# Performance work log

Measured on AMD Instinct MI355X. Metric: run time of the kernel, lower is better.

Reference implementation:

```python
import jax, jax.numpy as jnp
import numpy as np

B, H, W, R, C = 4, 64, 64, 64, 32  # batch, height, width, in-channels r, conv out-channels


def setup_inputs() -> dict:
    key = jax.random.key(0)
    kx, kf, kg = jax.random.split(key, 3)
    x = jax.random.normal(kx, (B, H, W, R), dtype=jnp.float32)
    # 1x1 conv with in_channels=1: kernel is effectively a length-C vector
    w_f = jax.random.normal(kf, (C,), dtype=jnp.float32) * 0.1
    w_g = jax.random.normal(kg, (C,), dtype=jnp.float32) * 0.1
    gamma = jnp.ones((), dtype=jnp.float32)
    return {"x": x, "w_f": w_f, "w_g": w_g, "gamma": gamma}


def reference(x, w_f, w_g, gamma):
    b, h, w, r = x.shape
    hw = h * w
    xs = x.reshape(b, hw, r)                      # [B, HW, R]
    # conv_f / conv_g: each scalar of xs times weight vector -> [B, HW, R*C]
    x_f = (xs[..., None] * w_f).reshape(b, hw, -1)
    x_g = (xs[..., None] * w_g).reshape(b, hw, -1)
    attn = jnp.einsum('bik,bjk->bij', x_f, x_g)   # [B, HW, HW]
    attn = jax.nn.softmax(attn, axis=-1) * gamma
    # out[b,j,r] = sum_i attn[b,j,i] * xs[b,i,r]
    out = jnp.einsum('bji,bir->bjr', attn, xs)
    return out.reshape(b, h, w, r)
```

## Files before the change

### kernel.cpp

```cpp
#include <hip/hip_runtime.h>


#define N_SEQ 4096
#define KS    4
#define LOG2E 1.4426950408889634f
#define LDP2  72

typedef __attribute__((ext_vector_type(8))) short short8;
typedef __attribute__((ext_vector_type(4))) short short4v;
typedef __attribute__((ext_vector_type(4))) float f4;
typedef _Float16 half8  __attribute__((ext_vector_type(8)));
typedef _Float16 half4v __attribute__((ext_vector_type(4)));
typedef _Float16 half2t __attribute__((ext_vector_type(2)));
typedef __fp16   fp16x2 __attribute__((ext_vector_type(2)));

union U8  { short8 v8; short4v v4[2]; unsigned short u[8]; };
union HU8 { half8 v; half2t h2[4]; unsigned short u[8]; };
union HU4 { half4v v; half2t h2[2]; unsigned short u[4]; };
union PK  { fp16x2 f; half2t h; };

#define MFMA16(a,b,c) __builtin_amdgcn_mfma_f32_16x16x32_bf16(a,b,c,0,0,0)
#define MFMAH(a,b,c)  __builtin_amdgcn_mfma_f32_16x16x32_f16(a,b,c,0,0,0)

static __device__ __forceinline__ unsigned short f2bf(float f){
  unsigned int u = __float_as_uint(f);
  u += 0x7fffu + ((u>>16)&1u);
  return (unsigned short)(u>>16);
}
static __device__ __forceinline__ float bf2f(unsigned short b){
  return __uint_as_float(((unsigned int)b)<<16);
}
static __device__ __forceinline__ half2t pkrtz(float a, float b){
#if __has_builtin(__builtin_amdgcn_cvt_pkrtz)
  PK u; u.f = __builtin_amdgcn_cvt_pkrtz(a, b);
  return u.h;
#else
  half2t r; r.x = (_Float16)a; r.y = (_Float16)b; return r;
#endif
}
static __device__ __forceinline__ float fexp2(float x){
#if __has_builtin(__builtin_amdgcn_exp2f)
  return __builtin_amdgcn_exp2f(x);
#else
  return exp2f(x);
#endif
}
static __device__ __forceinline__ f4 splat4(float v){ f4 r; r.x=v; r.y=v; r.z=v; r.w=v; return r; }
static __device__ __forceinline__ f4 exp2v(f4 v){
  f4 r; r.x=fexp2(v.x); r.y=fexp2(v.y); r.z=fexp2(v.z); r.w=fexp2(v.w); return r;
}
static __device__ __forceinline__ f4 max4(f4 a, f4 b){
  f4 r; r.x=fmaxf(a.x,b.x); r.y=fmaxf(a.y,b.y); r.z=fmaxf(a.z,b.z); r.w=fmaxf(a.w,b.w); return r;
}
static __device__ __forceinline__ f4 shx4(f4 v, int m){
  f4 r; r.x=__shfl_xor(v.x,m,64); r.y=__shfl_xor(v.y,m,64);
        r.z=__shfl_xor(v.z,m,64); r.w=__shfl_xor(v.w,m,64); return r;
}
static __device__ __forceinline__ void gld_lds16(const void* g, void* l){
  __builtin_amdgcn_global_load_lds(
      (const __attribute__((address_space(1))) unsigned int*)g,
      (__attribute__((address_space(3))) unsigned int*)l, 16, 0, 0);
}

__global__ __launch_bounds__(256) void prep_kernel(
    const float* __restrict__ x, unsigned short* __restrict__ xh,
    unsigned short* __restrict__ xt)
{
  __shared__ unsigned short T[64][66];
  const int tid = threadIdx.x;
  const int bb  = blockIdx.x >> 6;
  const int n0  = (blockIdx.x & 63) << 6;
  {
    const int r  = tid >> 2;
    const int c4 = tid & 3;
    const float* src = x + ((size_t)(bb*N_SEQ + n0 + r))*64 + c4*16;
    unsigned short h[16];
    #pragma unroll
    for (int i = 0; i < 4; ++i) {
      const float4 f = *(const float4*)(src + i*4);
      HU4 u; u.h2[0] = pkrtz(f.x, f.y); u.h2[1] = pkrtz(f.z, f.w);
      h[i*4+0]=u.u[0]; h[i*4+1]=u.u[1]; h[i*4+2]=u.u[2]; h[i*4+3]=u.u[3];
    }
    unsigned short* dst = xh + ((size_t)(bb*N_SEQ + n0 + r))*64 + c4*16;
    U8 u0, u1;
    #pragma unroll
    for (int j = 0; j < 8; ++j) { u0.u[j]=h[j]; u1.u[j]=h[8+j]; }
    *(short8*)dst = u0.v8; *(short8*)(dst+8) = u1.v8;
    #pragma unroll
    for (int j = 0; j < 16; ++j) T[r][c4*16+j] = h[j];
  }
  __syncthreads();
  {
    const int d = tid >> 2;
    const int g = tid & 3;
    unsigned short o[16];
    #pragma unroll
    for (int j = 0; j < 16; ++j) o[j] = T[g*16+j][d];
    unsigned short* dst = xt + ((size_t)(bb*64 + d))*N_SEQ + n0 + g*16;
    U8 u0, u1;
    #pragma unroll
    for (int j = 0; j < 8; ++j) { u0.u[j]=o[j]; u1.u[j]=o[8+j]; }
    *(short8*)dst = u0.v8; *(short8*)(dst+8) = u1.v8;
  }
}

__global__ __launch_bounds__(256, 3) void fattn2_kernel(
    const float* __restrict__ x, const float* __restrict__ wf,
    const float* __restrict__ wg,
    const unsigned short* __restrict__ xh, const unsigned short* __restrict__ xt,
    float* __restrict__ OP, float* __restrict__ LP)
{
  __shared__ __align__(16) unsigned short KH[2][4096];
  __shared__ __align__(16) unsigned short VT[2][4096];
  __shared__ __align__(16) unsigned short PB[4][32*LDP2];

  const int tid  = threadIdx.x;
  const int lane = tid & 63;
  const int wv   = tid >> 6;
  const int mg   = wv & 1;
  const int hh   = wv >> 1;
  const int quad = lane >> 4;
  const int l15  = lane & 15;
  const int swz  = l15 & 7;
  const int ks   = blockIdx.x >> 8;
  const int rem  = blockIdx.x & 255;
  const int bb   = rem >> 6;
  const int qb   = (rem & 63) << 6;

  float s = 0.f;
  #pragma unroll
  for (int i = 0; i < 32; ++i) s += wf[i]*wg[i];
  const float s2 = s * LOG2E;

  const float* xb = x + ((size_t)bb * N_SEQ) * 64;

  half8 qf[2][2];
  #pragma unroll
  for (int mt = 0; mt < 2; ++mt) {
    const int row = qb + mg*32 + mt*16 + l15;
    #pragma unroll
    for (int c = 0; c < 2; ++c) {
      const float* src = xb + row*64 + c*32 + quad*8;
      const float4 a0 = *(const float4*)src;
      const float4 a1 = *(const float4*)(src+4);
      HU8 u;
      u.h2[0] = pkrtz(a0.x*s2, a0.y*s2);
      u.h2[1] = pkrtz(a0.z*s2, a0.w*s2);
      u.h2[2] = pkrtz(a1.x*s2, a1.y*s2);
      u.h2[3] = pkrtz(a1.z*s2, a1.w*s2);
      qf[mt][c] = u.v;
    }
  }

  f4 Oc[2][4];
  f4 lsa[2];
  #pragma unroll
  for (int mt = 0; mt < 2; ++mt) {
    lsa[mt] = splat4(0.f);
    #pragma unroll
    for (int nt = 0; nt < 4; ++nt) Oc[mt][nt] = splat4(0.f);
  }

  const int kbb = ks*1024;
  unsigned short* PBw = PB[wv];

  #pragma unroll 1
  for (int t = 0; t < 8; ++t) {
    const int kt = kbb + t*64;
    #pragma unroll
    for (int i = 0; i < 8; ++i) {
      const int reg = i >> 1;
      const int h   = reg & 1;
      const int ch  = wv*2 + (i & 1);
      const int p   = ch*64 + lane;
      const int rr  = p >> 3;
      const int cg  = (p & 7) ^ (rr & 7);
      if (reg < 2) {
        gld_lds16(xh + ((size_t)(bb*N_SEQ + kt + h*512 + rr))*64 + cg*8, &KH[h][ch*512]);
      } else {
        gld_lds16(xt + ((size_t)(bb*64 + rr))*N_SEQ + (kt + h*512 + cg*8), &VT[h][ch*512]);
      }
    }
    __syncthreads();

    f4 St[4][2];
    #pragma unroll
    for (int k2 = 0; k2 < 4; ++k2)
      #pragma unroll
      for (int mt = 0; mt < 2; ++mt) St[k2][mt] = splat4(0.f);

    #pragma unroll
    for (int c = 0; c < 2; ++c) {
      half8 kf[4];
      #pragma unroll
      for (int k2 = 0; k2 < 4; ++k2)
        kf[k2] = *(const half8*)&KH[hh][(k2*16 + l15)*64 + (((c*4 + quad) ^ swz))*8];
      #pragma unroll
      for (int k2 = 0; k2 < 4; ++k2)
        #pragma unroll
        for (int mt = 0; mt < 2; ++mt)
          St[k2][mt] = MFMAH(kf[k2], qf[mt][c], St[k2][mt]);
    }

    #pragma unroll
    for (int k2 = 0; k2 < 4; ++k2) {
      #pragma unroll
      for (int mt = 0; mt < 2; ++mt) {
        const f4 p = exp2v(St[k2][mt]);
        lsa[mt] += p;
        HU4 u; u.h2[0] = pkrtz(p.x, p.y); u.h2[1] = pkrtz(p.z, p.w);
        *(half4v*)&PBw[(mt*16 + l15)*LDP2 + k2*16 + quad*4] = u.v;
      }
    }

    #pragma unroll
    for (int kc = 0; kc < 2; ++kc) {
      half8 pa[2];
      #pragma unroll
      for (int mt = 0; mt < 2; ++mt)
        pa[mt] = *(const half8*)&PBw[(mt*16 + l15)*LDP2 + kc*32 + quad*8];
      #pragma unroll
      for (int nt = 0; nt < 4; ++nt) {
        const half8 vb = *(const half8*)&VT[hh][(nt*16 + l15)*64 + (((kc*4 + quad) ^ swz))*8];
        #pragma unroll
        for (int mt = 0; mt < 2; ++mt)
          Oc[mt][nt] = MFMAH(pa[mt], vb, Oc[mt][nt]);
      }
    }
    __syncthreads();
  }

  float lsum[2];
  #pragma unroll
  for (int mt = 0; mt < 2; ++mt) {
    float sv = lsa[mt].x + lsa[mt].y + lsa[mt].z + lsa[mt].w;
    sv += __shfl_xor(sv, 16, 64);
    sv += __shfl_xor(sv, 32, 64);
    lsum[mt] = sv;
  }

  float* MO = (float*)KH;
  float* ML = (float*)VT;
  if (hh == 1) {
    #pragma unroll
    for (int mt = 0; mt < 2; ++mt) {
      const int rbase = mg*32 + mt*16 + quad*4;
      #pragma unroll
      for (int nt = 0; nt < 4; ++nt) {
        MO[(rbase+0)*64 + nt*16 + l15] = Oc[mt][nt].x;
        MO[(rbase+1)*64 + nt*16 + l15] = Oc[mt][nt].y;
        MO[(rbase+2)*64 + nt*16 + l15] = Oc[mt][nt].z;
        MO[(rbase+3)*64 + nt*16 + l15] = Oc[mt][nt].w;
      }
      if (quad == 0) ML[mg*32 + mt*16 + l15] = lsum[mt];
    }
  }
  __syncthreads();
  if (hh == 0) {
    float* op = OP + (size_t)blockIdx.x * 4096;
    #pragma unroll
    for (int mt = 0; mt < 2; ++mt) {
      const int rbase = mg*32 + mt*16 + quad*4;
      #pragma unroll
      for (int nt = 0; nt < 4; ++nt) {
        #pragma unroll
        for (int rg = 0; rg < 4; ++rg) {
          const int rr = rbase + rg;
          op[rr*64 + nt*16 + l15] = Oc[mt][nt][rg] + MO[rr*64 + nt*16 + l15];
        }
      }
      if (quad == 0)
        LP[(size_t)blockIdx.x*64 + mg*32 + mt*16 + l15] = lsum[mt] + ML[mg*32 + mt*16 + l15];
    }
  }
}

__global__ __launch_bounds__(256) void merge_kernel(
    const float* __restrict__ OP, const float* __restrict__ LP,
    const float* __restrict__ gm, float* __restrict__ out)
{
  const int idx = blockIdx.x*256 + threadIdx.x;
  const int e0  = idx*4;
  const int d0  = e0 & 63;
  const int row = e0 >> 6;
  const int bb  = row >> 12;
  const int q   = row & 4095;
  const int qt  = q >> 6;
  const int qr  = q & 63;
  float4 acc = make_float4(0.f,0.f,0.f,0.f);
  float l = 0.f;
  #pragma unroll
  for (int sct = 0; sct < KS; ++sct) {
    const int blk = sct*256 + bb*64 + qt;
    const float4 o = *(const float4*)(OP + (size_t)blk*4096 + qr*64 + d0);
    acc.x += o.x; acc.y += o.y; acc.z += o.z; acc.w += o.w;
    l += LP[(size_t)blk*64 + qr];
  }
  const float w = gm[0] / l;
  float4 r; r.x = acc.x*w; r.y = acc.y*w; r.z = acc.z*w; r.w = acc.w*w;
  *(float4*)(out + e0) = r;
}

#define LDKF 72
#define TILEF (64*LDKF)
#define LDP 36

__global__ __launch_bounds__(256) void fattn_fallback(
    const float* __restrict__ x, const float* __restrict__ wf,
    const float* __restrict__ wg, const float* __restrict__ gm,
    float* __restrict__ out)
{
  __shared__ __align__(16) unsigned short KHI[2*TILEF];
  __shared__ __align__(16) unsigned short KLO[2*TILEF];
  __shared__ __align__(16) unsigned short VT [2*TILEF];
  __shared__ __align__(16) unsigned short PB [4*32*LDP];

  const int tid  = threadIdx.x;
  const int lane = tid & 63;
  const int wv   = tid >> 6;
  const int mg   = wv & 1;
  const int hh   = wv >> 1;
  const int quad = lane >> 4;
  const int l15  = lane & 15;
  const int bb   = blockIdx.x >> 6;
  const int qb   = (blockIdx.x & 63) << 6;

  float s = 0.f;
  #pragma unroll
  for (int i = 0; i < 32; ++i) s += wf[i]*wg[i];
  const float s2 = s * LOG2E;
  const float gamma = gm[0];

  const float* xb = x + ((size_t)bb * N_SEQ) * 64;

  short8 qhf[2][2], qlf[2][2];
  #pragma unroll
  for (int mt = 0; mt < 2; ++mt) {
    const int row = qb + mg*32 + mt*16 + l15;
    #pragma unroll
    for (int c = 0; c < 2; ++c) {
      const float* src = xb + row*64 + c*32 + quad*8;
      const float4 a0 = *(const float4*)src;
      const float4 a1 = *(const float4*)(src+4);
      float qv[8] = {a0.x,a0.y,a0.z,a0.w,a1.x,a1.y,a1.z,a1.w};
      U8 vh, vl;
      #pragma unroll
      for (int j = 0; j < 8; ++j) {
        float q = qv[j]*s2;
        unsigned short hb = f2bf(q);
        vh.u[j] = (short)hb;
        vl.u[j] = (short)f2bf(q - bf2f(hb));
      }
      qhf[mt][c] = vh.v8; qlf[mt][c] = vl.v8;
    }
  }

  f4 Oc[2][4], mo[2], ls[2];
  #pragma unroll
  for (int mt = 0; mt < 2; ++mt) {
    mo[mt] = splat4(-1e30f);
    ls[mt] = splat4(0.f);
    #pragma unroll
    for (int nt = 0; nt < 4; ++nt) Oc[mt][nt] = splat4(0.f);
  }

  const int sh   = tid >> 7;
  const int srow = (tid & 127) >> 1;
  const int sch  = tid & 1;

  float4 sr[8];
  {
    const float* sp = xb + (sh*2048 + srow)*64 + sch*32;
    #pragma unroll
    for (int i = 0; i < 8; ++i) sr[i] = *(const float4*)(sp + i*4);
    unsigned short hb[32], lb[32];
    #pragma unroll
    for (int i = 0; i < 8; ++i) {
      float vv[4] = {sr[i].x, sr[i].y, sr[i].z, sr[i].w};
      #pragma unroll
      for (int j = 0; j < 4; ++j) {
        unsigned short h = f2bf(vv[j]);
        hb[i*4+j] = h;
        lb[i*4+j] = f2bf(vv[j] - bf2f(h));
      }
    }
    const int kbase = sh*TILEF + srow*LDKF + sch*32;
    #pragma unroll
    for (int g = 0; g < 4; ++g) {
      U8 wh, wl;
      #pragma unroll
      for (int j = 0; j < 8; ++j) { wh.u[j]=(short)hb[g*8+j]; wl.u[j]=(short)lb[g*8+j]; }
      *(short8*)&KHI[kbase+g*8] = wh.v8;
      *(short8*)&KLO[kbase+g*8] = wl.v8;
    }
    #pragma unroll
    for (int j = 0; j < 32; ++j) VT[sh*TILEF + (sch*32+j)*LDKF + srow] = hb[j];
  }
  __syncthreads();

  #pragma unroll 1
  for (int t = 0; t < 32; ++t) {
    if (t+1 < 32) {
      const float* sp = xb + (sh*2048 + (t+1)*64 + srow)*64 + sch*32;
      #pragma unroll
      for (int i = 0; i < 8; ++i) sr[i] = *(const float4*)(sp + i*4);
    }

    f4 Sa[2][4];
    #pragma unroll
    for (int mt = 0; mt < 2; ++mt)
      #pragma unroll
      for (int n = 0; n < 4; ++n) Sa[mt][n] = splat4(0.f);

    const int kldsb = hh*TILEF;
    #pragma unroll
    for (int n = 0; n < 4; ++n) {
      #pragma unroll
      for (int c = 0; c < 2; ++c) {
        const int off = kldsb + (n*16 + l15)*LDKF + c*32 + quad*8;
        const short8 bh = *(const short8*)&KHI[off];
        const short8 bl = *(const short8*)&KLO[off];
        #pragma unroll
        for (int mt = 0; mt < 2; ++mt) {
          Sa[mt][n] = MFMA16(qhf[mt][c], bh, Sa[mt][n]);
          Sa[mt][n] = MFMA16(qlf[mt][c], bh, Sa[mt][n]);
          Sa[mt][n] = MFMA16(qhf[mt][c], bl, Sa[mt][n]);
        }
      }
    }

    f4 p[2][4];
    #pragma unroll
    for (int mt = 0; mt < 2; ++mt) {
      f4 rm = max4(max4(Sa[mt][0],Sa[mt][1]), max4(Sa[mt][2],Sa[mt][3]));
      rm = max4(rm, shx4(rm,1));
      rm = max4(rm, shx4(rm,2));
      rm = max4(rm, shx4(rm,4));
      rm = max4(rm, shx4(rm,8));
      f4 mn = max4(mo[mt], rm);
      f4 al = exp2v(mo[mt] - mn);
      mo[mt] = mn;
      f4 rs = splat4(0.f);
      #pragma unroll
      for (int n = 0; n < 4; ++n) { p[mt][n] = exp2v(Sa[mt][n] - mn); rs += p[mt][n]; }
      rs += shx4(rs,1); rs += shx4(rs,2); rs += shx4(rs,4); rs += shx4(rs,8);
      ls[mt] = ls[mt]*al + rs;
      #pragma unroll
      for (int nt = 0; nt < 4; ++nt) Oc[mt][nt] *= al;
    }

    const int pw = wv * (32*LDP);
    #pragma unroll
    for (int kc = 0; kc < 2; ++kc) {
      #pragma unroll
      for (int mt = 0; mt < 2; ++mt) {
        #pragma unroll
        for (int n2 = 0; n2 < 2; ++n2) {
          const f4 pv = p[mt][kc*2+n2];
          const int base = pw + (mt*16 + quad*4)*LDP + n2*16 + l15;
          ((unsigned short*)PB)[base        ] = f2bf(pv.x);
          ((unsigned short*)PB)[base +   LDP] = f2bf(pv.y);
          ((unsigned short*)PB)[base + 2*LDP] = f2bf(pv.z);
          ((unsigned short*)PB)[base + 3*LDP] = f2bf(pv.w);
        }
      }
      short8 pa[2];
      #pragma unroll
      for (int mt = 0; mt < 2; ++mt) {
        U8 u;
        const int rb = pw + (mt*16 + l15)*LDP + quad*8;
        u.v4[0] = *(const short4v*)&((unsigned short*)PB)[rb];
        u.v4[1] = *(const short4v*)&((unsigned short*)PB)[rb+4];
        pa[mt] = u.v8;
      }
      #pragma unroll
      for (int nt = 0; nt < 4; ++nt) {
        const short8 vb = *(const short8*)&VT[kldsb + (nt*16 + l15)*LDKF + kc*32 + quad*8];
        #pragma unroll
        for (int mt = 0; mt < 2; ++mt) Oc[mt][nt] = MFMA16(pa[mt], vb, Oc[mt][nt]);
      }
    }

    __syncthreads();

    if (t+1 < 32) {
      unsigned short hb[32], lb[32];
      #pragma unroll
      for (int i = 0; i < 8; ++i) {
        float vv[4] = {sr[i].x, sr[i].y, sr[i].z, sr[i].w};
        #pragma unroll
        for (int j = 0; j < 4; ++j) {
          unsigned short h = f2bf(vv[j]);
          hb[i*4+j] = h;
          lb[i*4+j] = f2bf(vv[j] - bf2f(h));
        }
      }
      const int kbase = sh*TILEF + srow*LDKF + sch*32;
      #pragma unroll
      for (int g = 0; g < 4; ++g) {
        U8 wh, wl;
        #pragma unroll
        for (int j = 0; j < 8; ++j) { wh.u[j]=(short)hb[g*8+j]; wl.u[j]=(short)lb[g*8+j]; }
        *(short8*)&KHI[kbase+g*8] = wh.v8;
        *(short8*)&KLO[kbase+g*8] = wl.v8;
      }
      #pragma unroll
      for (int j = 0; j < 32; ++j) VT[sh*TILEF + (sch*32+j)*LDKF + srow] = hb[j];
      __syncthreads();
    }
  }

  float* MO  = (float*)KHI;
  float* MML = (float*)KLO;
  if (hh == 1) {
    #pragma unroll
    for (int mt = 0; mt < 2; ++mt) {
      const int rbase = mg*32 + mt*16 + quad*4;
      #pragma unroll
      for (int nt = 0; nt < 4; ++nt) {
        MO[(rbase+0)*64 + nt*16 + l15] = Oc[mt][nt].x;
        MO[(rbase+1)*64 + nt*16 + l15] = Oc[mt][nt].y;
        MO[(rbase+2)*64 + nt*16 + l15] = Oc[mt][nt].z;
        MO[(rbase+3)*64 + nt*16 + l15] = Oc[mt][nt].w;
      }
      if (l15 == 0) {
        MML[rbase+0] = mo[mt].x; MML[rbase+1] = mo[mt].y;
        MML[rbase+2] = mo[mt].z; MML[rbase+3] = mo[mt].w;
        MML[64+rbase+0] = ls[mt].x; MML[64+rbase+1] = ls[mt].y;
        MML[64+rbase+2] = ls[mt].z; MML[64+rbase+3] = ls[mt].w;
      }
    }
  }
  __syncthreads();
  if (hh == 0) {
    #pragma unroll
    for (int mt = 0; mt < 2; ++mt) {
      const int rbase = mg*32 + mt*16 + quad*4;
      f4 m1, l1;
      m1.x = MML[rbase+0]; m1.y = MML[rbase+1]; m1.z = MML[rbase+2]; m1.w = MML[rbase+3];
      l1.x = MML[64+rbase+0]; l1.y = MML[64+rbase+1]; l1.z = MML[64+rbase+2]; l1.w = MML[64+rbase+3];
      const f4 mn = max4(mo[mt], m1);
      const f4 a0 = exp2v(mo[mt] - mn);
      const f4 a1 = exp2v(m1 - mn);
      f4 lt = ls[mt]*a0 + l1*a1;
      f4 w; w.x = gamma/lt.x; w.y = gamma/lt.y; w.z = gamma/lt.z; w.w = gamma/lt.w;
      #pragma unroll
      for (int nt = 0; nt < 4; ++nt) {
        #pragma unroll
        for (int rg = 0; rg < 4; ++rg) {
          const int rr = rbase + rg;
          const float o1 = MO[rr*64 + nt*16 + l15];
          const float val = (Oc[mt][nt][rg]*a0[rg] + o1*a1[rg]) * w[rg];
          out[((size_t)bb*N_SEQ + qb + rr)*64 + nt*16 + l15] = val;
        }
      }
    }
  }
}

extern "C" void kernel_launch(void* const* d_in, const int* in_sizes, int n_in,
                              void* d_out, int out_size, void* d_ws, size_t ws_size,
                              hipStream_t stream) {
  const float* x  = (const float*)d_in[0];
  const float* wf = (const float*)d_in[1];
  const float* wg = (const float*)d_in[2];
  const float* gm = (const float*)d_in[3];
  float* out = (float*)d_out;

  const size_t XH_OFF = 0;
  const size_t XT_OFF = 2097152;
  const size_t OP_OFF = 4194304;
  const size_t LP_OFF = 20971520;
  const size_t NEED   = 21233664;

  if (ws_size >= NEED) {
    unsigned short* xhp = (unsigned short*)((char*)d_ws + XH_OFF);
    unsigned short* xtp = (unsigned short*)((char*)d_ws + XT_OFF);
    float* OP = (float*)((char*)d_ws + OP_OFF);
    float* LP = (float*)((char*)d_ws + LP_OFF);
    prep_kernel<<<dim3(256), dim3(256), 0, stream>>>(x, xhp, xtp);
    fattn2_kernel<<<dim3(KS*256), dim3(256), 0, stream>>>(x, wf, wg, xhp, xtp, OP, LP);
    merge_kernel<<<dim3(1024), dim3(256), 0, stream>>>(OP, LP, gm, out);
  } else {
    fattn_fallback<<<dim3(256), dim3(256), 0, stream>>>(x, wf, wg, gm, out);
  }
}
```

Before: 97.98 us.

## Use three-way uneven key split with register-staged prefetch of K/V tiles

Reduces the key-sequence split from 4 to 3 partitions (22/21/21 tiles of 64 keys), so the grid is 768 blocks. At 3 blocks per CU that matches a single wave on the device, removing the tail wave. The direct global-to-LDS loads are replaced by a register-staged double buffer: the next pair of K/V tiles is loaded into registers while the current pair is computed, then stored to LDS at the top of the next iteration. The odd tile count leaves one wave-half idle on the last iteration. Register staging also adds VGPR pressure and extra LDS store instructions.

```diff
diff --git a/kernel.cpp b/kernel.cpp
--- a/kernel.cpp
+++ b/kernel.cpp
@@ -2,7 +2,7 @@
 
 
 #define N_SEQ 4096
-#define KS    4
+#define KS    3
 #define LOG2E 1.4426950408889634f
 #define LDP2  72
 
@@ -55,11 +55,6 @@
 static __device__ __forceinline__ f4 shx4(f4 v, int m){
   f4 r; r.x=__shfl_xor(v.x,m,64); r.y=__shfl_xor(v.y,m,64);
         r.z=__shfl_xor(v.z,m,64); r.w=__shfl_xor(v.w,m,64); return r;
-}
-static __device__ __forceinline__ void gld_lds16(const void* g, void* l){
-  __builtin_amdgcn_global_load_lds(
-      (const __attribute__((address_space(1))) unsigned int*)g,
-      (__attribute__((address_space(3))) unsigned int*)l, 16, 0, 0);
 }
 
 __global__ __launch_bounds__(256) void prep_kernel(
@@ -104,7 +99,7 @@
   }
 }
 
-__global__ __launch_bounds__(256, 3) void fattn2_kernel(
+__global__ __launch_bounds__(256, 3) void fattn3_kernel(
     const float* __restrict__ x, const float* __restrict__ wf,
     const float* __restrict__ wg,
     const unsigned short* __restrict__ xh, const unsigned short* __restrict__ xt,
@@ -127,6 +122,10 @@
   const int bb   = rem >> 6;
   const int qb   = (rem & 63) << 6;
 
+  const int t0 = (ks == 0) ? 0 : (22 + 21*(ks-1));
+  const int t1 = t0 + ((ks == 0) ? 22 : 21);
+  const int NIT = 11;
+
   float s = 0.f;
   #pragma unroll
   for (int i = 0; i < 32; ++i) s += wf[i]*wg[i];
@@ -161,70 +160,99 @@
     for (int nt = 0; nt < 4; ++nt) Oc[mt][nt] = splat4(0.f);
   }
 
-  const int kbb = ks*1024;
   unsigned short* PBw = PB[wv];
 
+  int srr[8], scg[8];
+  #pragma unroll
+  for (int i = 0; i < 8; ++i) {
+    const int ch = wv*2 + (i & 1);
+    const int p  = ch*64 + lane;
+    srr[i] = p >> 3;
+    scg[i] = (p & 7) ^ (srr[i] & 7);
+  }
+
+  short8 sr[8];
+
+  #pragma unroll
+  for (int i = 0; i < 8; ++i) {
+    const int h   = (i >> 1) & 1;
+    const int tIx = min(t0 + h, t1 - 1);
+    const int kg  = tIx * 64;
+    if ((i >> 1) < 2)
+      sr[i] = *(const short8*)(xh + ((size_t)(bb*N_SEQ + kg + srr[i]))*64 + scg[i]*8);
+    else
+      sr[i] = *(const short8*)(xt + ((size_t)(bb*64 + srr[i]))*N_SEQ + kg + scg[i]*8);
+  }
+
   #pragma unroll 1
-  for (int t = 0; t < 8; ++t) {
-    const int kt = kbb + t*64;
+  for (int it = 0; it < NIT; ++it) {
     #pragma unroll
     for (int i = 0; i < 8; ++i) {
-      const int reg = i >> 1;
-      const int h   = reg & 1;
-      const int ch  = wv*2 + (i & 1);
-      const int p   = ch*64 + lane;
-      const int rr  = p >> 3;
-      const int cg  = (p & 7) ^ (rr & 7);
-      if (reg < 2) {
-        gld_lds16(xh + ((size_t)(bb*N_SEQ + kt + h*512 + rr))*64 + cg*8, &KH[h][ch*512]);
-      } else {
-        gld_lds16(xt + ((size_t)(bb*64 + rr))*N_SEQ + (kt + h*512 + cg*8), &VT[h][ch*512]);
-      }
+      const int ch = wv*2 + (i & 1);
+      const int p  = ch*64 + lane;
+      unsigned short* base = ((i >> 1) < 2) ? &KH[(i>>1)&1][0] : &VT[(i>>1)&1][0];
+      *(short8*)(base + p*8) = sr[i];
     }
     __syncthreads();
 
-    f4 St[4][2];
-    #pragma unroll
-    for (int k2 = 0; k2 < 4; ++k2)
-      #pragma unroll
-      for (int mt = 0; mt < 2; ++mt) St[k2][mt] = splat4(0.f);
-
-    #pragma unroll
-    for (int c = 0; c < 2; ++c) {
-      half8 kf[4];
+    if (it + 1 < NIT) {
+      #pragma unroll
+      for (int i = 0; i < 8; ++i) {
+        const int h   = (i >> 1) & 1;
+        const int tIx = min(t0 + (it+1)*2 + h, t1 - 1);
+        const int kg  = tIx * 64;
+        if ((i >> 1) < 2)
+          sr[i] = *(const short8*)(xh + ((size_t)(bb*N_SEQ + kg + srr[i]))*64 + scg[i]*8);
+        else
+          sr[i] = *(const short8*)(xt + ((size_t)(bb*64 + srr[i]))*N_SEQ + kg + scg[i]*8);
+      }
+    }
+
+    const bool valid = (t0 + it*2 + hh) < t1;
+    if (valid) {
+      f4 St[4][2];
       #pragma unroll
       for (int k2 = 0; k2 < 4; ++k2)
-        kf[k2] = *(const half8*)&KH[hh][(k2*16 + l15)*64 + (((c*4 + quad) ^ swz))*8];
-      #pragma unroll
-      for (int k2 = 0; k2 < 4; ++k2)
+        #pragma unroll
+        for (int mt = 0; mt < 2; ++mt) St[k2][mt] = splat4(0.f);
+
+      #pragma unroll
+      for (int c = 0; c < 2; ++c) {
+        half8 kf[4];
+        #pragma unroll
+        for (int k2 = 0; k2 < 4; ++k2)
+          kf[k2] = *(const half8*)&KH[hh][(k2*16 + l15)*64 + (((c*4 + quad) ^ swz))*8];
+        #pragma unroll
+        for (int k2 = 0; k2 < 4; ++k2)
+          #pragma unroll
+          for (int mt = 0; mt < 2; ++mt)
+            St[k2][mt] = MFMAH(kf[k2], qf[mt][c], St[k2][mt]);
+      }
+
+      #pragma unroll
+      for (int k2 = 0; k2 < 4; ++k2) {
+        #pragma unroll
+        for (int mt = 0; mt < 2; ++mt) {
+          const f4 p = exp2v(St[k2][mt]);
+          lsa[mt] += p;
+          HU4 u; u.h2[0] = pkrtz(p.x, p.y); u.h2[1] = pkrtz(p.z, p.w);
+          *(half4v*)&PBw[(mt*16 + l15)*LDP2 + k2*16 + quad*4] = u.v;
+        }
+      }
+
+      #pragma unroll
+      for (int kc = 0; kc < 2; ++kc) {
+        half8 pa[2];
         #pragma unroll
         for (int mt = 0; mt < 2; ++mt)
-          St[k2][mt] = MFMAH(kf[k2], qf[mt][c], St[k2][mt]);
-    }
-
-    #pragma unroll
-    for (int k2 = 0; k2 < 4; ++k2) {
-      #pragma unroll
-      for (int mt = 0; mt < 2; ++mt) {
-        const f4 p = exp2v(St[k2][mt]);
-        lsa[mt] += p;
-        HU4 u; u.h2[0] = pkrtz(p.x, p.y); u.h2[1] = pkrtz(p.z, p.w);
-        *(half4v*)&PBw[(mt*16 + l15)*LDP2 + k2*16 + quad*4] = u.v;
-      }
-    }
-
-    #pragma unroll
-    for (int kc = 0; kc < 2; ++kc) {
-      half8 pa[2];
-      #pragma unroll
-      for (int mt = 0; mt < 2; ++mt)
-        pa[mt] = *(const half8*)&PBw[(mt*16 + l15)*LDP2 + kc*32 + quad*8];
-      #pragma unroll
-      for (int nt = 0; nt < 4; ++nt) {
-        const half8 vb = *(const half8*)&VT[hh][(nt*16 + l15)*64 + (((kc*4 + quad) ^ swz))*8];
-        #pragma unroll
-        for (int mt = 0; mt < 2; ++mt)
-          Oc[mt][nt] = MFMAH(pa[mt], vb, Oc[mt][nt]);
+          pa[mt] = *(const half8*)&PBw[(mt*16 + l15)*LDP2 + kc*32 + quad*8];
+        #pragma unroll
+        for (int nt = 0; nt < 4; ++nt) {
+          const half8 vb = *(const half8*)&VT[hh][(nt*16 + l15)*64 + (((kc*4 + quad) ^ swz))*8];
+          #pragma unroll
+          for (int mt = 0; mt < 2; ++mt)
+            Oc[mt][nt] = MFMAH(pa[mt], vb, Oc[mt][nt]);
+        }
       }
     }
     __syncthreads();
@@ -570,8 +598,8 @@
   const size_t XH_OFF = 0;
   const size_t XT_OFF = 2097152;
   const size_t OP_OFF = 4194304;
-  const size_t LP_OFF = 20971520;
-  const size_t NEED   = 21233664;
+  const size_t LP_OFF = OP_OFF + (size_t)KS*256*4096*4;
+  const size_t NEED   = LP_OFF + (size_t)KS*256*64*4;
 
   if (ws_size >= NEED) {
     unsigned short* xhp = (unsigned short*)((char*)d_ws + XH_OFF);
@@ -579,7 +607,7 @@
     float* OP = (float*)((char*)d_ws + OP_OFF);
     float* LP = (float*)((char*)d_ws + LP_OFF);
     prep_kernel<<<dim3(256), dim3(256), 0, stream>>>(x, xhp, xtp);
-    fattn2_kernel<<<dim3(KS*256), dim3(256), 0, stream>>>(x, wf, wg, xhp, xtp, OP, LP);
+    fattn3_kernel<<<dim3(KS*256), dim3(256), 0, stream>>>(x, wf, wg, xhp, xtp, OP, LP);
     merge_kernel<<<dim3(1024), dim3(256), 0, stream>>>(OP, LP, gm, out);
   } else {
     fattn_fallback<<<dim3(256), dim3(256), 0, stream>>>(x, wf, wg, gm, out);
```

Result: faster. 96.03 us (-2.0%).
